# Performance work log

Measured on AMD Instinct MI355X. Metric: run time of the kernel, lower is better.

The kernel has to match this reference:

```python
import jax, jax.numpy as jnp
import numpy as np

B, D, N0, N1 = 2, 512, 2048, 2048
ATT_DIM, OUT_DIM, H = 512, 512, 8
HEAD_ATT = ATT_DIM // H   # 64
HEAD_OUT = OUT_DIM // H   # 64
TEMP = 1.0
MASK_FILL = -10000000.0


def setup_inputs() -> dict:
    key = jax.random.key(0)
    ks = jax.random.split(key, 12)
    s = 0.02
    return {
        "feats_query": jax.random.normal(ks[0], (B, D, N0), dtype=jnp.float32),
        "feats_key": jax.random.normal(ks[1], (B, D, N1), dtype=jnp.float32),
        "key_mask": jax.random.randint(ks[2], (B, 1, N1), 0, 2, dtype=jnp.int32),
        # 1x1 Conv1d weights == (out_ch, in_ch) matrices
        "Wq": jax.random.normal(ks[3], (ATT_DIM, D), dtype=jnp.float32) * s,
        "bq": jnp.zeros((ATT_DIM,), dtype=jnp.float32),
        "Wk": jax.random.normal(ks[4], (ATT_DIM, D), dtype=jnp.float32) * s,
        "bk": jnp.zeros((ATT_DIM,), dtype=jnp.float32),
        "Wf": jax.random.normal(ks[5], (OUT_DIM, D), dtype=jnp.float32) * s,
        "bf": jnp.zeros((OUT_DIM,), dtype=jnp.float32),
        "Wm": jax.random.normal(ks[6], (OUT_DIM, OUT_DIM), dtype=jnp.float32) * s,
        "bm": jnp.zeros((OUT_DIM,), dtype=jnp.float32),
        "ln_g": jnp.ones((OUT_DIM,), dtype=jnp.float32),
        "ln_b": jnp.zeros((OUT_DIM,), dtype=jnp.float32),
    }


def _conv1x1(W, b, x):  # x: (b, in, n) -> (b, out, n)
    return jnp.einsum('oi,bin->bon', W, x) + b[None, :, None]


def reference(feats_query, feats_key, key_mask, Wq, bq, Wk, bk, Wf, bf, Wm, bm, ln_g, ln_b):
    b = feats_query.shape[0]
    n0 = feats_query.shape[2]
    n1 = feats_key.shape[2]
    # projections; channel split is (head_dim, head_num) per torch reshape
    q = _conv1x1(Wq, bq, feats_query).reshape(b, HEAD_ATT, H, n0)
    k = _conv1x1(Wk, bk, feats_key).reshape(b, HEAD_ATT, H, n1)
    v = _conv1x1(Wf, bf, feats_key).reshape(b, HEAD_OUT, H, n1)
    # attention: scores scaled by head_att_dim ** 0.5 (dim = query.shape[1])
    scores = jnp.einsum('bdhn,bdhm->bhnm', q / TEMP, k) / (HEAD_ATT ** 0.5)
    mask = key_mask.reshape(b, 1, 1, n1)
    scores = jnp.where(mask == 0, MASK_FILL, scores)
    prob = jax.nn.softmax(scores, axis=-1)
    feats_out = jnp.einsum('bhnm,bdhm->bdhn', prob, v).reshape(b, HEAD_OUT * H, n0)
    feats_out = _conv1x1(Wm, bm, feats_out)
    feats_out = feats_out + feats_query  # skip connection
    # SpecialLayerNorm: layernorm over channel dim (permute 0,2,1 -> LN -> permute back)
    x = feats_out.transpose(0, 2, 1)  # (b, n0, c)
    mu = jnp.mean(x, axis=-1, keepdims=True)
    var = jnp.var(x, axis=-1, keepdims=True)
    x = (x - mu) / jnp.sqrt(var + 1e-5) * ln_g + ln_b
    return x.transpose(0, 2, 1)  # (b, c, n0)
```

## Files before the change

### kernel.cpp

```cpp
#include <hip/hip_runtime.h>
#include <hip/hip_bf16.h>


using bf16x8 = __attribute__((ext_vector_type(8))) __bf16;
using f32x4  = __attribute__((ext_vector_type(4))) float;
using f32x16 = __attribute__((ext_vector_type(16))) float;
using us8    = __attribute__((ext_vector_type(8))) unsigned short;
using u32x4  = __attribute__((ext_vector_type(4))) unsigned int;

__device__ __forceinline__ unsigned short f2b(float f) {
  unsigned int u = __builtin_bit_cast(unsigned int, f);
  u += 0x7fffu + ((u >> 16) & 1u);
  return (unsigned short)(u >> 16);
}
__device__ __forceinline__ float b2f(unsigned short s) {
  unsigned int u = ((unsigned int)s) << 16;
  return __builtin_bit_cast(float, u);
}
__device__ __forceinline__ unsigned int cvtpk(float lo, float hi) {
  unsigned int w;
  asm("v_cvt_pk_bf16_f32 %0, %1, %2" : "=v"(w) : "v"(lo), "v"(hi));
  return w;
}
__device__ __forceinline__ void gl_lds16(const void* g, void* l) {
  __builtin_amdgcn_global_load_lds((const __attribute__((address_space(1))) void*)g,
                                   (__attribute__((address_space(3))) void*)l, 16, 0, 0);
}

__global__ __launch_bounds__(256) void k_pre(
    const float* __restrict__ fq, const float* __restrict__ fk,
    const float* __restrict__ Wq, const float* __restrict__ Wk,
    const float* __restrict__ Wf, const float* __restrict__ Wm,
    const int* __restrict__ mask,
    unsigned short* __restrict__ xqt, unsigned short* __restrict__ xkt,
    unsigned short* __restrict__ wqb, unsigned short* __restrict__ wkb,
    unsigned short* __restrict__ wfb, unsigned short* __restrict__ wmb,
    float* __restrict__ biasf)
{
  const int id = blockIdx.x;
  const int t = threadIdx.x;
  __shared__ float tile[64][65];

  if (id < 1024) {
    const int which = id >> 9;
    const int b = (id >> 8) & 1;
    const int i0 = ((id >> 5) & 7) * 64;
    const int n0 = (id & 31) * 64;
    const float* __restrict__ src = which ? fk : fq;
    unsigned short* __restrict__ dst = which ? xkt : xqt;
    const int cl = t & 63, rw = t >> 6;
    #pragma unroll
    for (int rr = 0; rr < 16; ++rr) {
      int il = rr * 4 + rw;
      tile[il][cl] = src[((size_t)b * 512 + i0 + il) * 2048 + n0 + cl];
    }
    __syncthreads();
    const int ci = (t & 31) * 2, rhalf = t >> 5;
    #pragma unroll
    for (int rr = 0; rr < 8; ++rr) {
      int nl = rr * 8 + rhalf;
      unsigned int v = (unsigned int)f2b(tile[ci][nl]) |
                       ((unsigned int)f2b(tile[ci + 1][nl]) << 16);
      *(unsigned int*)&dst[((size_t)b * 2048 + n0 + nl) * 512 + i0 + ci] = v;
    }
  } else if (id < 3072) {
    const int r = id - 1024;
    const int mat = r >> 9, cp = r & 511;
    if (mat < 3) {
      const float* W = (mat == 0) ? Wq : (mat == 1) ? Wk : Wf;
      unsigned short* O = (mat == 0) ? wqb : (mat == 1) ? wkb : wfb;
      const int orig = (cp & 63) * 8 + (cp >> 6);
      for (int j = t; j < 512; j += 256)
        O[cp * 512 + j] = f2b(W[orig * 512 + j]);
    } else {
      for (int j = t; j < 512; j += 256) {
        int h = j >> 6, d = j & 63;
        wmb[cp * 512 + j] = f2b(Wm[cp * 512 + d * 8 + h]);
      }
    }
  } else {
    const int r = id - 3072;
    if (r < 16) {
      int i = r * 256 + t;
      biasf[i] = mask[i] ? 0.f : -100000.f;
    }
  }
}

__global__ __launch_bounds__(256) void k_proj(
    const unsigned short* __restrict__ xqt, const unsigned short* __restrict__ xkt,
    const unsigned short* __restrict__ wqp, const unsigned short* __restrict__ wkp,
    const unsigned short* __restrict__ wfp,
    const float* __restrict__ bq, const float* __restrict__ bk, const float* __restrict__ bfv,
    unsigned short* __restrict__ Qb, unsigned short* __restrict__ Kb, unsigned short* __restrict__ VTb)
{
  const int lid = blockIdx.x;
  const int orig = (lid & 7) * 48 + (lid >> 3);
  const int z = orig >> 6;
  const int bid = orig & 63;
  const int b = z / 3, proj = z % 3;
  const int t = threadIdx.x, w = t >> 6, l = t & 63, q = l >> 4, m16 = l & 15;
  const int wm = w >> 1, wn = w & 1;

  __shared__ __attribute__((aligned(16))) unsigned short As[2][8192];
  __shared__ __attribute__((aligned(16))) unsigned short Bs[2][8192];

  const unsigned short* A;
  const unsigned short* Bt;
  int mt, nt_;
  if (proj < 2) {
    mt = bid >> 2; nt_ = bid & 3;
    A  = (proj == 0 ? xqt : xkt) + (size_t)b * 2048 * 512 + (size_t)mt * 128 * 512;
    Bt = (proj == 0 ? wqp : wkp) + (size_t)nt_ * 128 * 512;
  } else {
    mt = bid & 3; nt_ = bid >> 2;
    A  = wfp + (size_t)mt * 128 * 512;
    Bt = xkt + (size_t)b * 2048 * 512 + (size_t)nt_ * 128 * 512;
  }

  f32x4 acc[4][4];
  const f32x4 fz = {0.f, 0.f, 0.f, 0.f};
  #pragma unroll
  for (int mf = 0; mf < 4; ++mf)
    #pragma unroll
    for (int nf = 0; nf < 4; ++nf) acc[mf][nf] = fz;

#define PROJ_STAGE(BUF, KS)                                                          \
  {                                                                                  \
    _Pragma("unroll")                                                                \
    for (int c = 0; c < 4; ++c) {                                                    \
      int slot = c * 256 + t;                                                        \
      int row = slot >> 3, j = slot & 7;                                             \
      int jj = j ^ (row & 7);                                                        \
      gl_lds16(A  + (size_t)row * 512 + (KS) * 64 + jj * 8,                          \
               (char*)As[BUF] + (c * 256 + w * 64) * 16);                            \
      gl_lds16(Bt + (size_t)row * 512 + (KS) * 64 + jj * 8,                          \
               (char*)Bs[BUF] + (c * 256 + w * 64) * 16);                            \
    }                                                                                \
  }

  PROJ_STAGE(0, 0)
  asm volatile("s_waitcnt vmcnt(0)" ::: "memory");
  __syncthreads();

  for (int ks = 0; ks < 8; ++ks) {
    const int cur = ks & 1;
    if (ks < 7) PROJ_STAGE(cur ^ 1, ks + 1)
    #pragma unroll
    for (int kk = 0; kk < 2; ++kk) {
      bf16x8 av[4], bv[4];
      #pragma unroll
      for (int mf = 0; mf < 4; ++mf) {
        int row = wm * 64 + mf * 16 + m16;
        av[mf] = *(const bf16x8*)&As[cur][row * 64 + (((kk * 4 + q) ^ (row & 7)) << 3)];
      }
      #pragma unroll
      for (int nf = 0; nf < 4; ++nf) {
        int row = wn * 64 + nf * 16 + m16;
        bv[nf] = *(const bf16x8*)&Bs[cur][row * 64 + (((kk * 4 + q) ^ (row & 7)) << 3)];
      }
      #pragma unroll
      for (int mf = 0; mf < 4; ++mf)
        #pragma unroll
        for (int nf = 0; nf < 4; ++nf)
          acc[mf][nf] = __builtin_amdgcn_mfma_f32_16x16x32_bf16(av[mf], bv[nf], acc[mf][nf], 0, 0, 0);
    }
    if (ks < 7) {
      asm volatile("s_waitcnt vmcnt(0)" ::: "memory");
      __syncthreads();
    }
  }
#undef PROJ_STAGE

  const float QSCALE = 0.18033688011112042f;

  if (proj < 2) {
    const float* bias = (proj == 0) ? bq : bk;
    unsigned short* dst = (proj == 0) ? Qb : Kb;
    #pragma unroll
    for (int mf = 0; mf < 4; ++mf)
      #pragma unroll
      for (int nf = 0; nf < 4; ++nf)
        #pragma unroll
        for (int r = 0; r < 4; ++r) {
          int n  = mt * 128 + wm * 64 + mf * 16 + q * 4 + r;
          int cp = nt_ * 128 + wn * 64 + nf * 16 + m16;
          int h = cp >> 6, d = cp & 63;
          float v = acc[mf][nf][r] + bias[d * 8 + h];
          if (proj == 0) v *= QSCALE;
          dst[((size_t)(b * 8 + h) * 2048 + n) * 64 + d] = f2b(v);
        }
  } else {
    #pragma unroll
    for (int mf = 0; mf < 4; ++mf)
      #pragma unroll
      for (int nf = 0; nf < 4; ++nf)
        #pragma unroll
        for (int r = 0; r < 4; ++r) {
          int cp = mt * 128 + wm * 64 + mf * 16 + q * 4 + r;
          int n  = nt_ * 128 + wn * 64 + nf * 16 + m16;
          int h = cp >> 6, d = cp & 63;
          float v = acc[mf][nf][r] + bfv[d * 8 + h];
          VTb[((size_t)(b * 8 + h) * 64 + d) * 2048 + n] = f2b(v);
        }
  }
}

__global__ __launch_bounds__(256, 2) void k_attn4(
    const unsigned short* __restrict__ Qb, const unsigned short* __restrict__ Kb,
    const unsigned short* __restrict__ VTb, const float* __restrict__ biasf,
    unsigned short* __restrict__ OT)
{
  const int lid = blockIdx.x;
  const int orig = ((lid & 7) << 6) | (lid >> 3);
  const int bh = orig >> 5, b = bh >> 3, h = bh & 7;
  const int nt = orig & 31;
  const int t = threadIdx.x, w = t >> 6, l = t & 63;
  const int q31 = l & 31, hi = l >> 5;

  __shared__ __attribute__((aligned(16))) char lds_all[70656];

  const unsigned short* Kp = Kb + (size_t)bh * (2048 * 64);
  const unsigned short* Vp = VTb + (size_t)bh * (64 * 2048);
  const float* brow = biasf + b * 2048;

  bf16x8 qfr[2][4];
  {
    const unsigned short* Qp = Qb + ((size_t)bh * 2048 + nt * 64) * 64;
    #pragma unroll
    for (int qf = 0; qf < 2; ++qf)
      #pragma unroll
      for (int tq = 0; tq < 4; ++tq)
        qfr[qf][tq] = *(const bf16x8*)&Qp[(qf * 32 + q31) * 64 + tq * 16 + hi * 8];
  }

  f32x16 z16;
  #pragma unroll
  for (int r = 0; r < 16; ++r) z16[r] = 0.f;
  f32x16 oacc[2][2];
  oacc[0][0] = z16; oacc[0][1] = z16; oacc[1][0] = z16; oacc[1][1] = z16;
  float lpart[2] = {0.f, 0.f};

  auto LK = [&](int i, bf16x8 (&kk)[4], bf16x8 (&vv)[4]) {
    const int kv0 = (w + 4 * i) * 32;
    #pragma unroll
    for (int tq = 0; tq < 4; ++tq)
      kk[tq] = *(const bf16x8*)&Kp[(size_t)(kv0 + q31) * 64 + tq * 16 + hi * 8];
    #pragma unroll
    for (int df = 0; df < 2; ++df)
      #pragma unroll
      for (int tt = 0; tt < 2; ++tt)
        vv[df * 2 + tt] = *(const bf16x8*)&Vp[(size_t)(df * 32 + q31) * 2048 + kv0 + tt * 16 + hi * 8];
  };

  auto COMPUTE = [&](int i, bf16x8 (&kk)[4], bf16x8 (&vv)[4]) {
    const int kv0 = (w + 4 * i) * 32;
    float4 bias[4];
    #pragma unroll
    for (int g = 0; g < 4; ++g)
      bias[g] = *(const float4*)&brow[kv0 + g * 8 + hi * 4];

    #pragma unroll
    for (int qf = 0; qf < 2; ++qf) {
      f32x16 sacc;
      __builtin_amdgcn_s_setprio(1);
      sacc = __builtin_amdgcn_mfma_f32_32x32x16_bf16(kk[0], qfr[qf][0], z16, 0, 0, 0);
      #pragma unroll
      for (int tq = 1; tq < 4; ++tq)
        sacc = __builtin_amdgcn_mfma_f32_32x32x16_bf16(kk[tq], qfr[qf][tq], sacc, 0, 0, 0);
      __builtin_amdgcn_s_setprio(0);

      float e[16];
      #pragma unroll
      for (int g = 0; g < 4; ++g) {
        e[g*4+0] = __builtin_amdgcn_exp2f(sacc[g*4+0] + bias[g].x);
        e[g*4+1] = __builtin_amdgcn_exp2f(sacc[g*4+1] + bias[g].y);
        e[g*4+2] = __builtin_amdgcn_exp2f(sacc[g*4+2] + bias[g].z);
        e[g*4+3] = __builtin_amdgcn_exp2f(sacc[g*4+3] + bias[g].w);
      }
      {
        float s0 = e[0]+e[1], s1 = e[2]+e[3], s2 = e[4]+e[5], s3 = e[6]+e[7];
        float s4 = e[8]+e[9], s5 = e[10]+e[11], s6 = e[12]+e[13], s7 = e[14]+e[15];
        float t0 = s0+s1, t1 = s2+s3, t2 = s4+s5, t3 = s6+s7;
        lpart[qf] += (t0+t1) + (t2+t3);
      }

      unsigned int W[8];
      #pragma unroll
      for (int j = 0; j < 8; ++j) W[j] = cvtpk(e[2*j], e[2*j+1]);
      asm("v_permlane32_swap_b32 %0, %1" : "+v"(W[0]), "+v"(W[2]));
      asm("v_permlane32_swap_b32 %0, %1" : "+v"(W[1]), "+v"(W[3]));
      asm("v_permlane32_swap_b32 %0, %1" : "+v"(W[4]), "+v"(W[6]));
      asm("v_permlane32_swap_b32 %0, %1" : "+v"(W[5]), "+v"(W[7]));
      u32x4 lo4 = {W[0], W[1], W[2], W[3]};
      u32x4 hi4 = {W[4], W[5], W[6], W[7]};
      bf16x8 pb0 = __builtin_bit_cast(bf16x8, lo4);
      bf16x8 pb1 = __builtin_bit_cast(bf16x8, hi4);

      __builtin_amdgcn_s_setprio(1);
      oacc[0][qf] = __builtin_amdgcn_mfma_f32_32x32x16_bf16(vv[0], pb0, oacc[0][qf], 0, 0, 0);
      oacc[0][qf] = __builtin_amdgcn_mfma_f32_32x32x16_bf16(vv[1], pb1, oacc[0][qf], 0, 0, 0);
      oacc[1][qf] = __builtin_amdgcn_mfma_f32_32x32x16_bf16(vv[2], pb0, oacc[1][qf], 0, 0, 0);
      oacc[1][qf] = __builtin_amdgcn_mfma_f32_32x32x16_bf16(vv[3], pb1, oacc[1][qf], 0, 0, 0);
      __builtin_amdgcn_s_setprio(0);
    }
  };

  bf16x8 kA[4], vA[4], kB[4], vB[4];
  LK(0, kA, vA);
  for (int ii = 0; ii < 8; ++ii) {
    LK(2 * ii + 1, kB, vB);
    COMPUTE(2 * ii, kA, vA);
    if (ii < 7) LK(2 * ii + 2, kA, vA);
    COMPUTE(2 * ii + 1, kB, vB);
  }

  float* pc = (float*)lds_all;
  float* ls = (float*)(lds_all + 69632);
  #pragma unroll
  for (int qf = 0; qf < 2; ++qf) {
    float lfull = lpart[qf] + __shfl_xor(lpart[qf], 32);
    int qq = qf * 32 + q31;
    if (hi == 0) ls[w * 64 + qq] = lfull;
    #pragma unroll
    for (int df = 0; df < 2; ++df)
      #pragma unroll
      for (int g = 0; g < 4; ++g) {
        f32x4 v4 = {oacc[df][qf][g*4+0], oacc[df][qf][g*4+1],
                    oacc[df][qf][g*4+2], oacc[df][qf][g*4+3]};
        *(f32x4*)&pc[w * 4352 + qq * 68 + df * 32 + g * 8 + hi * 4] = v4;
      }
  }
  __syncthreads();
  {
    const int q = t >> 2, ds = (t & 3) * 16;
    float lsumv = ls[q] + ls[64 + q] + ls[128 + q] + ls[192 + q];
    f32x4 o4[4];
    #pragma unroll
    for (int j = 0; j < 4; ++j) o4[j] = *(const f32x4*)&pc[q * 68 + ds + j * 4];
    #pragma unroll
    for (int ww = 1; ww < 4; ++ww)
      #pragma unroll
      for (int j = 0; j < 4; ++j) {
        f32x4 p4 = *(const f32x4*)&pc[ww * 4352 + q * 68 + ds + j * 4];
        o4[j] += p4;
      }
    float rinv = __builtin_amdgcn_rcpf(lsumv);
    unsigned int pk[8];
    #pragma unroll
    for (int j = 0; j < 4; ++j) {
      pk[2*j]   = cvtpk(o4[j][0] * rinv, o4[j][1] * rinv);
      pk[2*j+1] = cvtpk(o4[j][2] * rinv, o4[j][3] * rinv);
    }
    unsigned short* dst = &OT[((size_t)b * 2048 + nt * 64 + q) * 512 + h * 64 + ds];
    u32x4 s0 = {pk[0], pk[1], pk[2], pk[3]};
    u32x4 s1 = {pk[4], pk[5], pk[6], pk[7]};
    *(u32x4*)dst = s0;
    *(u32x4*)(dst + 8) = s1;
  }
}

__global__ __launch_bounds__(256) void k_out(
    const unsigned short* __restrict__ OT, const unsigned short* __restrict__ wmw,
    const float* __restrict__ bm, const float* __restrict__ fq,
    const float* __restrict__ g, const float* __restrict__ be,
    float* __restrict__ out)
{
  const int b = blockIdx.y;
  const int n0 = blockIdx.x * 32;
  const int t = threadIdx.x, w = t >> 6, l = t & 63, q = l >> 4, m16 = l & 15;

  __shared__ __attribute__((aligned(16))) unsigned short As[2][2048];
  __shared__ __attribute__((aligned(16))) unsigned short Bs[2][32768];
  __shared__ float ssum[4][32], ssq[4][32];

  f32x4 acc[2][8];
  const f32x4 fz = {0.f, 0.f, 0.f, 0.f};
  #pragma unroll
  for (int mf = 0; mf < 2; ++mf)
    #pragma unroll
    for (int nf = 0; nf < 8; ++nf) acc[mf][nf] = fz;

  const unsigned short* Abase = OT + ((size_t)b * 2048 + n0) * 512;
  const unsigned short* Bbase = wmw;

#define OUT_STAGE(BUF, KS)                                                          \
  {                                                                                 \
    { int row = t >> 3, j = t & 7;                                                  \
      gl_lds16(Abase + (size_t)row * 512 + (KS) * 64 + ((j ^ (row & 7)) * 8),       \
               (char*)As[BUF] + w * 1024); }                                        \
    _Pragma("unroll")                                                               \
    for (int c = 0; c < 16; ++c) {                                                  \
      int slot = c * 256 + t;                                                       \
      int row = slot >> 3, j = slot & 7;                                            \
      gl_lds16(Bbase + (size_t)row * 512 + (KS) * 64 + ((j ^ (row & 7)) * 8),       \
               (char*)Bs[BUF] + (c * 256 + w * 64) * 16);                           \
    }                                                                               \
  }

  OUT_STAGE(0, 0)
  asm volatile("s_waitcnt vmcnt(0)" ::: "memory");
  __syncthreads();

  for (int ks = 0; ks < 8; ++ks) {
    const int cur = ks & 1;
    if (ks < 7) OUT_STAGE(cur ^ 1, ks + 1)
    #pragma unroll
    for (int kk = 0; kk < 2; ++kk) {
      bf16x8 av[2];
      #pragma unroll
      for (int mf = 0; mf < 2; ++mf) {
        int row = mf * 16 + m16;
        av[mf] = *(const bf16x8*)((const char*)As[cur] + row * 128 + (((kk * 4 + q) ^ (row & 7)) * 16));
      }
      #pragma unroll
      for (int nf = 0; nf < 8; ++nf) {
        int row = w * 128 + nf * 16 + m16;
        bf16x8 bv = *(const bf16x8*)((const char*)Bs[cur] + row * 128 + (((kk * 4 + q) ^ (row & 7)) * 16));
        acc[0][nf] = __builtin_amdgcn_mfma_f32_16x16x32_bf16(av[0], bv, acc[0][nf], 0, 0, 0);
        acc[1][nf] = __builtin_amdgcn_mfma_f32_16x16x32_bf16(av[1], bv, acc[1][nf], 0, 0, 0);
      }
    }
    if (ks < 7) {
      asm volatile("s_waitcnt vmcnt(0)" ::: "memory");
      __syncthreads();
    }
  }
#undef OUT_STAGE

  float gv[8], bev[8], bmv[8];
  #pragma unroll
  for (int nf = 0; nf < 8; ++nf) {
    int c = w * 128 + nf * 16 + m16;
    gv[nf] = g[c]; bev[nf] = be[c]; bmv[nf] = bm[c];
  }
  #pragma unroll
  for (int mf = 0; mf < 2; ++mf)
    #pragma unroll
    for (int nf = 0; nf < 8; ++nf) {
      int c = w * 128 + nf * 16 + m16;
      f32x4 res = *(const f32x4*)&fq[((size_t)b * 512 + c) * 2048 + n0 + mf * 16 + q * 4];
      #pragma unroll
      for (int r = 0; r < 4; ++r)
        acc[mf][nf][r] += bmv[nf] + res[r];
    }
  #pragma unroll
  for (int mf = 0; mf < 2; ++mf)
    #pragma unroll
    for (int r = 0; r < 4; ++r) {
      float ps = 0.f, pss = 0.f;
      #pragma unroll
      for (int nf = 0; nf < 8; ++nf) {
        float v = acc[mf][nf][r];
        ps += v; pss += v * v;
      }
      ps += __shfl_xor(ps, 1); pss += __shfl_xor(pss, 1);
      ps += __shfl_xor(ps, 2); pss += __shfl_xor(pss, 2);
      ps += __shfl_xor(ps, 4); pss += __shfl_xor(pss, 4);
      ps += __shfl_xor(ps, 8); pss += __shfl_xor(pss, 8);
      if (m16 == 0) {
        ssum[w][mf * 16 + q * 4 + r] = ps;
        ssq[w][mf * 16 + q * 4 + r] = pss;
      }
    }
  __syncthreads();
  #pragma unroll
  for (int mf = 0; mf < 2; ++mf)
    #pragma unroll
    for (int r = 0; r < 4; ++r) {
      int nl = mf * 16 + q * 4 + r;
      float S  = ssum[0][nl] + ssum[1][nl] + ssum[2][nl] + ssum[3][nl];
      float SS = ssq[0][nl] + ssq[1][nl] + ssq[2][nl] + ssq[3][nl];
      float mu = S * (1.f / 512.f);
      float var = SS * (1.f / 512.f) - mu * mu;
      float rstd = rsqrtf(var + 1e-5f);
      #pragma unroll
      for (int nf = 0; nf < 8; ++nf)
        acc[mf][nf][r] = (acc[mf][nf][r] - mu) * rstd * gv[nf] + bev[nf];
    }
  #pragma unroll
  for (int mf = 0; mf < 2; ++mf)
    #pragma unroll
    for (int nf = 0; nf < 8; ++nf) {
      int c = w * 128 + nf * 16 + m16;
      *(f32x4*)&out[((size_t)b * 512 + c) * 2048 + n0 + mf * 16 + q * 4] = acc[mf][nf];
    }
}

extern "C" void kernel_launch(void* const* d_in, const int* in_sizes, int n_in,
                              void* d_out, int out_size, void* d_ws, size_t ws_size,
                              hipStream_t stream) {
  const float* fq  = (const float*)d_in[0];
  const float* fk  = (const float*)d_in[1];
  const int*   msk = (const int*)d_in[2];
  const float* Wq  = (const float*)d_in[3];
  const float* bq  = (const float*)d_in[4];
  const float* Wk  = (const float*)d_in[5];
  const float* bk  = (const float*)d_in[6];
  const float* Wf  = (const float*)d_in[7];
  const float* bfv = (const float*)d_in[8];
  const float* Wm  = (const float*)d_in[9];
  const float* bm  = (const float*)d_in[10];
  const float* lng = (const float*)d_in[11];
  const float* lnb = (const float*)d_in[12];
  float* out = (float*)d_out;

  char* ws = (char*)d_ws;
  const size_t MB = 1024 * 1024;
  unsigned short* xqt = (unsigned short*)(ws + 0 * MB);
  unsigned short* xkt = (unsigned short*)(ws + 4 * MB);
  unsigned short* wqb = (unsigned short*)(ws + 8 * MB);
  unsigned short* wkb = (unsigned short*)(ws + 8 * MB + 512 * 1024);
  unsigned short* wfb = (unsigned short*)(ws + 9 * MB);
  unsigned short* wmb = (unsigned short*)(ws + 9 * MB + 512 * 1024);
  unsigned short* Qb  = (unsigned short*)(ws + 10 * MB);
  unsigned short* Kb  = (unsigned short*)(ws + 14 * MB);
  unsigned short* VTb = (unsigned short*)(ws + 18 * MB);
  unsigned short* OTb = (unsigned short*)(ws + 22 * MB);
  float*          biasf = (float*)(ws + 26 * MB);

  hipLaunchKernelGGL(k_pre, dim3(3088), dim3(256), 0, stream,
                     fq, fk, Wq, Wk, Wf, Wm, msk, xqt, xkt, wqb, wkb, wfb, wmb, biasf);
  hipLaunchKernelGGL(k_proj, dim3(384), dim3(256), 0, stream,
                     xqt, xkt, wqb, wkb, wfb, bq, bk, bfv, Qb, Kb, VTb);
  hipLaunchKernelGGL(k_attn4, dim3(512), dim3(256), 0, stream, Qb, Kb, VTb, biasf, OTb);
  hipLaunchKernelGGL(k_out, dim3(64, 2), dim3(256), 0, stream,
                     OTb, wmb, bm, fq, lng, lnb, out);
}
```

Before: 83.91 us.

## Bit-pack key mask and hand-schedule attention loads with inline asm waitcnt

The float bias array for the key mask becomes a packed bitmask built in the pre-kernel, and the attention kernel zeroes masked exp values with bit tests instead of loading float4 bias per chunk. K/V/Q loads are issued through inline-asm global_load_dwordx4 with immediate offsets and pointer increments. Explicit vmcnt waits and sched barriers give a manual double-buffered prefetch. This cuts bias memory traffic and address arithmetic but relies on exact vmcnt accounting. Masked exps are now exactly zero instead of exp2 of a large negative, so a fully masked row would divide by zero.

```diff
diff --git a/kernel.cpp b/kernel.cpp
--- a/kernel.cpp
+++ b/kernel.cpp
@@ -25,6 +25,13 @@
 __device__ __forceinline__ void gl_lds16(const void* g, void* l) {
   __builtin_amdgcn_global_load_lds((const __attribute__((address_space(1))) void*)g,
                                    (__attribute__((address_space(3))) void*)l, 16, 0, 0);
+}
+template <int OFF>
+__device__ __forceinline__ bf16x8 gload16(const unsigned short* p) {
+  u32x4 r;
+  asm volatile("global_load_dwordx4 %0, %1, off offset:%2"
+               : "=v"(r) : "v"(p), "i"(OFF) : "memory");
+  return __builtin_bit_cast(bf16x8, r);
 }
 
 __global__ __launch_bounds__(256) void k_pre(
@@ -35,7 +42,7 @@
     unsigned short* __restrict__ xqt, unsigned short* __restrict__ xkt,
     unsigned short* __restrict__ wqb, unsigned short* __restrict__ wkb,
     unsigned short* __restrict__ wfb, unsigned short* __restrict__ wmb,
-    float* __restrict__ biasf)
+    unsigned int* __restrict__ mbits)
 {
   const int id = blockIdx.x;
   const int t = threadIdx.x;
@@ -79,10 +86,13 @@
       }
     }
   } else {
-    const int r = id - 3072;
-    if (r < 16) {
-      int i = r * 256 + t;
-      biasf[i] = mask[i] ? 0.f : -100000.f;
+    if (t < 128) {
+      int bb = t >> 6, wd = t & 63;
+      unsigned int v = 0;
+      #pragma unroll
+      for (int j = 0; j < 32; ++j)
+        v |= (mask[bb * 2048 + wd * 32 + j] ? 1u : 0u) << j;
+      mbits[t] = v;
     }
   }
 }
@@ -206,9 +216,9 @@
   }
 }
 
-__global__ __launch_bounds__(256, 2) void k_attn4(
+__global__ __launch_bounds__(256, 2) void k_attn6(
     const unsigned short* __restrict__ Qb, const unsigned short* __restrict__ Kb,
-    const unsigned short* __restrict__ VTb, const float* __restrict__ biasf,
+    const unsigned short* __restrict__ VTb, const unsigned int* __restrict__ mbits,
     unsigned short* __restrict__ OT)
 {
   const int lid = blockIdx.x;
@@ -220,19 +230,19 @@
 
   __shared__ __attribute__((aligned(16))) char lds_all[70656];
 
-  const unsigned short* Kp = Kb + (size_t)bh * (2048 * 64);
-  const unsigned short* Vp = VTb + (size_t)bh * (64 * 2048);
-  const float* brow = biasf + b * 2048;
-
+  const unsigned int* mrow = mbits + b * 64;
+
+  const unsigned short* kptr = Kb + (size_t)bh * (2048 * 64) + (size_t)(w * 32 + q31) * 64 + hi * 8;
+  const unsigned short* v0ptr = VTb + (size_t)bh * (64 * 2048) + (size_t)q31 * 2048 + w * 32 + hi * 8;
+  const unsigned short* v1ptr = v0ptr + (size_t)32 * 2048;
+
+  const unsigned short* qp0 = Qb + ((size_t)bh * 2048 + nt * 64 + q31) * 64 + hi * 8;
+  const unsigned short* qp1 = qp0 + 32 * 64;
   bf16x8 qfr[2][4];
-  {
-    const unsigned short* Qp = Qb + ((size_t)bh * 2048 + nt * 64) * 64;
-    #pragma unroll
-    for (int qf = 0; qf < 2; ++qf)
-      #pragma unroll
-      for (int tq = 0; tq < 4; ++tq)
-        qfr[qf][tq] = *(const bf16x8*)&Qp[(qf * 32 + q31) * 64 + tq * 16 + hi * 8];
-  }
+  qfr[0][0] = gload16<0>(qp0);  qfr[0][1] = gload16<32>(qp0);
+  qfr[0][2] = gload16<64>(qp0); qfr[0][3] = gload16<96>(qp0);
+  qfr[1][0] = gload16<0>(qp1);  qfr[1][1] = gload16<32>(qp1);
+  qfr[1][2] = gload16<64>(qp1); qfr[1][3] = gload16<96>(qp1);
 
   f32x16 z16;
   #pragma unroll
@@ -241,79 +251,79 @@
   oacc[0][0] = z16; oacc[0][1] = z16; oacc[1][0] = z16; oacc[1][1] = z16;
   float lpart[2] = {0.f, 0.f};
 
-  auto LK = [&](int i, bf16x8 (&kk)[4], bf16x8 (&vv)[4]) {
-    const int kv0 = (w + 4 * i) * 32;
-    #pragma unroll
-    for (int tq = 0; tq < 4; ++tq)
-      kk[tq] = *(const bf16x8*)&Kp[(size_t)(kv0 + q31) * 64 + tq * 16 + hi * 8];
-    #pragma unroll
-    for (int df = 0; df < 2; ++df)
-      #pragma unroll
-      for (int tt = 0; tt < 2; ++tt)
-        vv[df * 2 + tt] = *(const bf16x8*)&Vp[(size_t)(df * 32 + q31) * 2048 + kv0 + tt * 16 + hi * 8];
-  };
-
-  auto COMPUTE = [&](int i, bf16x8 (&kk)[4], bf16x8 (&vv)[4]) {
-    const int kv0 = (w + 4 * i) * 32;
-    float4 bias[4];
-    #pragma unroll
-    for (int g = 0; g < 4; ++g)
-      bias[g] = *(const float4*)&brow[kv0 + g * 8 + hi * 4];
-
-    #pragma unroll
-    for (int qf = 0; qf < 2; ++qf) {
-      f32x16 sacc;
-      __builtin_amdgcn_s_setprio(1);
-      sacc = __builtin_amdgcn_mfma_f32_32x32x16_bf16(kk[0], qfr[qf][0], z16, 0, 0, 0);
-      #pragma unroll
-      for (int tq = 1; tq < 4; ++tq)
-        sacc = __builtin_amdgcn_mfma_f32_32x32x16_bf16(kk[tq], qfr[qf][tq], sacc, 0, 0, 0);
-      __builtin_amdgcn_s_setprio(0);
-
-      float e[16];
-      #pragma unroll
-      for (int g = 0; g < 4; ++g) {
-        e[g*4+0] = __builtin_amdgcn_exp2f(sacc[g*4+0] + bias[g].x);
-        e[g*4+1] = __builtin_amdgcn_exp2f(sacc[g*4+1] + bias[g].y);
-        e[g*4+2] = __builtin_amdgcn_exp2f(sacc[g*4+2] + bias[g].z);
-        e[g*4+3] = __builtin_amdgcn_exp2f(sacc[g*4+3] + bias[g].w);
-      }
-      {
-        float s0 = e[0]+e[1], s1 = e[2]+e[3], s2 = e[4]+e[5], s3 = e[6]+e[7];
-        float s4 = e[8]+e[9], s5 = e[10]+e[11], s6 = e[12]+e[13], s7 = e[14]+e[15];
-        float t0 = s0+s1, t1 = s2+s3, t2 = s4+s5, t3 = s6+s7;
-        lpart[qf] += (t0+t1) + (t2+t3);
-      }
-
-      unsigned int W[8];
-      #pragma unroll
-      for (int j = 0; j < 8; ++j) W[j] = cvtpk(e[2*j], e[2*j+1]);
-      asm("v_permlane32_swap_b32 %0, %1" : "+v"(W[0]), "+v"(W[2]));
-      asm("v_permlane32_swap_b32 %0, %1" : "+v"(W[1]), "+v"(W[3]));
-      asm("v_permlane32_swap_b32 %0, %1" : "+v"(W[4]), "+v"(W[6]));
-      asm("v_permlane32_swap_b32 %0, %1" : "+v"(W[5]), "+v"(W[7]));
-      u32x4 lo4 = {W[0], W[1], W[2], W[3]};
-      u32x4 hi4 = {W[4], W[5], W[6], W[7]};
-      bf16x8 pb0 = __builtin_bit_cast(bf16x8, lo4);
-      bf16x8 pb1 = __builtin_bit_cast(bf16x8, hi4);
-
-      __builtin_amdgcn_s_setprio(1);
-      oacc[0][qf] = __builtin_amdgcn_mfma_f32_32x32x16_bf16(vv[0], pb0, oacc[0][qf], 0, 0, 0);
-      oacc[0][qf] = __builtin_amdgcn_mfma_f32_32x32x16_bf16(vv[1], pb1, oacc[0][qf], 0, 0, 0);
-      oacc[1][qf] = __builtin_amdgcn_mfma_f32_32x32x16_bf16(vv[2], pb0, oacc[1][qf], 0, 0, 0);
-      oacc[1][qf] = __builtin_amdgcn_mfma_f32_32x32x16_bf16(vv[3], pb1, oacc[1][qf], 0, 0, 0);
-      __builtin_amdgcn_s_setprio(0);
-    }
-  };
+#define LOADCHUNK(KK, VV)                                                   \
+  {                                                                         \
+    KK[0] = gload16<0>(kptr);  KK[1] = gload16<32>(kptr);                   \
+    KK[2] = gload16<64>(kptr); KK[3] = gload16<96>(kptr);                   \
+    VV[0] = gload16<0>(v0ptr); VV[1] = gload16<32>(v0ptr);                  \
+    VV[2] = gload16<0>(v1ptr); VV[3] = gload16<32>(v1ptr);                  \
+    kptr += 8192; v0ptr += 128; v1ptr += 128;                               \
+  }
+
+#define COMPUTE(I, KK, VV)                                                            \
+  {                                                                                   \
+    const unsigned int mword = mrow[w + 4 * (I)];                                     \
+    const unsigned int mw2 = mword >> (hi * 4);                                       \
+    _Pragma("unroll")                                                                 \
+    for (int qf = 0; qf < 2; ++qf) {                                                  \
+      f32x16 sacc;                                                                    \
+      __builtin_amdgcn_s_setprio(1);                                                  \
+      sacc = __builtin_amdgcn_mfma_f32_32x32x16_bf16(KK[0], qfr[qf][0], z16, 0, 0, 0);\
+      sacc = __builtin_amdgcn_mfma_f32_32x32x16_bf16(KK[1], qfr[qf][1], sacc, 0, 0, 0);\
+      sacc = __builtin_amdgcn_mfma_f32_32x32x16_bf16(KK[2], qfr[qf][2], sacc, 0, 0, 0);\
+      sacc = __builtin_amdgcn_mfma_f32_32x32x16_bf16(KK[3], qfr[qf][3], sacc, 0, 0, 0);\
+      __builtin_amdgcn_s_setprio(0);                                                  \
+      float e[16];                                                                    \
+      _Pragma("unroll")                                                               \
+      for (int g = 0; g < 4; ++g)                                                     \
+        _Pragma("unroll")                                                             \
+        for (int r2 = 0; r2 < 4; ++r2) {                                              \
+          float ev = __builtin_amdgcn_exp2f(sacc[g * 4 + r2]);                        \
+          e[g * 4 + r2] = ((mw2 >> (r2 + 8 * g)) & 1u) ? ev : 0.f;                    \
+        }                                                                             \
+      {                                                                               \
+        float s0 = e[0]+e[1], s1 = e[2]+e[3], s2 = e[4]+e[5], s3 = e[6]+e[7];         \
+        float s4 = e[8]+e[9], s5 = e[10]+e[11], s6 = e[12]+e[13], s7 = e[14]+e[15];   \
+        lpart[qf] += ((s0+s1)+(s2+s3)) + ((s4+s5)+(s6+s7));                           \
+      }                                                                               \
+      unsigned int W[8];                                                              \
+      _Pragma("unroll")                                                               \
+      for (int j = 0; j < 8; ++j) W[j] = cvtpk(e[2*j], e[2*j+1]);                     \
+      asm("v_permlane32_swap_b32 %0, %1" : "+v"(W[0]), "+v"(W[2]));                   \
+      asm("v_permlane32_swap_b32 %0, %1" : "+v"(W[1]), "+v"(W[3]));                   \
+      asm("v_permlane32_swap_b32 %0, %1" : "+v"(W[4]), "+v"(W[6]));                   \
+      asm("v_permlane32_swap_b32 %0, %1" : "+v"(W[5]), "+v"(W[7]));                   \
+      u32x4 lo4 = {W[0], W[1], W[2], W[3]};                                           \
+      u32x4 hi4 = {W[4], W[5], W[6], W[7]};                                           \
+      bf16x8 pb0 = __builtin_bit_cast(bf16x8, lo4);                                   \
+      bf16x8 pb1 = __builtin_bit_cast(bf16x8, hi4);                                   \
+      __builtin_amdgcn_s_setprio(1);                                                  \
+      oacc[0][qf] = __builtin_amdgcn_mfma_f32_32x32x16_bf16(VV[0], pb0, oacc[0][qf], 0, 0, 0);\
+      oacc[0][qf] = __builtin_amdgcn_mfma_f32_32x32x16_bf16(VV[1], pb1, oacc[0][qf], 0, 0, 0);\
+      oacc[1][qf] = __builtin_amdgcn_mfma_f32_32x32x16_bf16(VV[2], pb0, oacc[1][qf], 0, 0, 0);\
+      oacc[1][qf] = __builtin_amdgcn_mfma_f32_32x32x16_bf16(VV[3], pb1, oacc[1][qf], 0, 0, 0);\
+      __builtin_amdgcn_s_setprio(0);                                                  \
+    }                                                                                 \
+  }
 
   bf16x8 kA[4], vA[4], kB[4], vB[4];
-  LK(0, kA, vA);
+  LOADCHUNK(kA, vA)
   for (int ii = 0; ii < 8; ++ii) {
-    LK(2 * ii + 1, kB, vB);
-    COMPUTE(2 * ii, kA, vA);
-    if (ii < 7) LK(2 * ii + 2, kA, vA);
-    COMPUTE(2 * ii + 1, kB, vB);
-  }
+    LOADCHUNK(kB, vB)
+    asm volatile("s_waitcnt vmcnt(8)" ::: "memory");
+    __builtin_amdgcn_sched_barrier(0);
+    COMPUTE(2 * ii, kA, vA)
+    if (ii < 7) {
+      LOADCHUNK(kA, vA)
+      asm volatile("s_waitcnt vmcnt(8)" ::: "memory");
+    } else {
+      asm volatile("s_waitcnt vmcnt(0)" ::: "memory");
+    }
+    __builtin_amdgcn_sched_barrier(0);
+    COMPUTE(2 * ii + 1, kB, vB)
+  }
+#undef LOADCHUNK
+#undef COMPUTE
 
   float* pc = (float*)lds_all;
   float* ls = (float*)(lds_all + 69632);
@@ -517,13 +527,13 @@
   unsigned short* Kb  = (unsigned short*)(ws + 14 * MB);
   unsigned short* VTb = (unsigned short*)(ws + 18 * MB);
   unsigned short* OTb = (unsigned short*)(ws + 22 * MB);
-  float*          biasf = (float*)(ws + 26 * MB);
-
-  hipLaunchKernelGGL(k_pre, dim3(3088), dim3(256), 0, stream,
-                     fq, fk, Wq, Wk, Wf, Wm, msk, xqt, xkt, wqb, wkb, wfb, wmb, biasf);
+  unsigned int*   mbits = (unsigned int*)(ws + 26 * MB);
+
+  hipLaunchKernelGGL(k_pre, dim3(3073), dim3(256), 0, stream,
+                     fq, fk, Wq, Wk, Wf, Wm, msk, xqt, xkt, wqb, wkb, wfb, wmb, mbits);
   hipLaunchKernelGGL(k_proj, dim3(384), dim3(256), 0, stream,
                      xqt, xkt, wqb, wkb, wfb, bq, bk, bfv, Qb, Kb, VTb);
-  hipLaunchKernelGGL(k_attn4, dim3(512), dim3(256), 0, stream, Qb, Kb, VTb, biasf, OTb);
+  hipLaunchKernelGGL(k_attn6, dim3(512), dim3(256), 0, stream, Qb, Kb, VTb, mbits, OTb);
   hipLaunchKernelGGL(k_out, dim3(64, 2), dim3(256), 0, stream,
                      OTb, wmb, bm, fq, lng, lnb, out);
 }
```

New measurement: 81.89 us. 2.4% less time.
